# Kernel tuning notes

Measured on AMD Instinct MI355X. Metric: run time of the kernel, lower is better.

## Reference

```python
import jax, jax.numpy as jnp
import numpy as np

B = 16384       # batch of weight blocks
IN = 64         # input_size == e_dim
DENC = 512      # dim_encoder
NRES = 2        # n_resblock (weights shared, see ResidualStack [block]*n)
NE = 2048       # n_embeddings
P = 12          # basis vectors per block
BETA = 0.25
SCALE = 1.0
SHIFT = 0.0


def setup_inputs() -> dict:
    key = jax.random.key(0)
    ks = jax.random.split(key, 6)
    s = 0.02
    return {
        "x": jax.random.normal(ks[0], (B, IN), dtype=jnp.float32),
        "enc_w1": jax.random.normal(ks[1], (IN, DENC), dtype=jnp.float32) * s,
        "enc_b1": jnp.zeros((DENC,), jnp.float32),
        "res_w": jax.random.normal(ks[2], (DENC, DENC), dtype=jnp.float32) * s,
        "res_b": jnp.zeros((DENC,), jnp.float32),
        "res_g": jnp.ones((DENC,), jnp.float32),
        "res_beta": jnp.zeros((DENC,), jnp.float32),
        "enc_w2": jax.random.normal(ks[3], (DENC, IN * P), dtype=jnp.float32) * s,
        "enc_b2": jnp.zeros((IN * P,), jnp.float32),
        "emb": jax.random.uniform(ks[4], (NE, IN), jnp.float32, -1.0 / NE, 1.0 / NE),
    }


def _layer_norm(r, g, b):
    mu = jnp.mean(r, axis=-1, keepdims=True)
    var = jnp.mean((r - mu) ** 2, axis=-1, keepdims=True)
    return (r - mu) * jax.lax.rsqrt(var + 1e-5) * g + b


def reference(x, enc_w1, enc_b1, res_w, res_b, res_g, res_beta, enc_w2, enc_b2, emb):
    sg = jax.lax.stop_gradient
    x_shift = (x - SHIFT) / SCALE

    # encoder: Linear -> (shared ResBlock) x NRES -> Linear
    h = x_shift @ enc_w1 + enc_b1                      # (B, DENC)
    for _ in range(NRES):
        h = h + jax.nn.relu(_layer_norm(h @ res_w + res_b, res_g, res_beta))
    z = h @ enc_w2 + enc_b2                            # (B, P*IN)

    z_e = z.reshape(B, P, IN)
    zf = z_e.reshape(-1, IN)                           # (B*P, IN)

    # pairwise squared distances to codebook, argmin, gather
    d = (jnp.sum(zf ** 2, axis=1, keepdims=True)
         + jnp.sum(emb ** 2, axis=1)
         - 2.0 * zf @ emb.T)                           # (B*P, NE)
    idx = jnp.argmin(d, axis=1)                        # (B*P,)
    z_q = emb[idx].reshape(B, P, IN)

    loss = (jnp.mean((sg(z_q) - z_e) ** 2)
            + BETA * jnp.mean((z_q - sg(z_e)) ** 2))

    # straight-through estimator
    z_q = z_e + sg(z_q - z_e)

    counts = jnp.zeros((NE,), jnp.float32).at[idx].add(1.0) / idx.shape[0]
    perplexity = jnp.exp(-jnp.sum(counts * jnp.log(counts + 1e-10)))

    # pinv-based reconstruction: A (B, IN, P), coeff = pinv(A) @ x_shift
    A = jnp.transpose(z_q, (0, 2, 1))                  # (B, IN, P)
    coeff = jnp.matmul(jnp.linalg.pinv(A), x_shift[..., None])  # (B, P, 1)
    x_hat = jnp.matmul(A, coeff)[..., 0]               # (B, IN)
    x_hat = SCALE * x_hat + SHIFT

    return (loss, x_hat, perplexity, idx, coeff)
```

## Files before the change

kernel.cpp:

```cpp
#include <hip/hip_runtime.h>
#include <math.h>

#define B_    16384
#define IN_   64
#define DENC_ 512
#define NE_   2048
#define P_    12
#define ROWS_ 196608
#define BETA_ 0.25

#define XHAT_OFF 1
#define PERP_OFF 1048577
#define IDXF_OFF 1048578
#define COEF_OFF 1245186

typedef __bf16 bf16x8 __attribute__((ext_vector_type(8)));
typedef float  f32x16 __attribute__((ext_vector_type(16)));

__device__ __forceinline__ void split3(float v, __bf16& h, __bf16& m, __bf16& l) {
    h = (__bf16)v;
    float r1 = v - (float)h;
    m = (__bf16)r1;
    float r2 = r1 - (float)m;
    l = (__bf16)r2;
}

__device__ __forceinline__ void gload_lds16(const void* g, void* l) {
    __builtin_amdgcn_global_load_lds((const __attribute__((address_space(1))) void*)g,
                                     (__attribute__((address_space(3))) void*)l, 16, 0, 0);
}

__global__ void k_wsplit(const float* __restrict__ W,
                         __bf16* __restrict__ Wh, __bf16* __restrict__ Wm,
                         __bf16* __restrict__ Wl, int kshift, int N, int total) {
    int idx = blockIdx.x * 256 + threadIdx.x;
    if (idx < total) {
        int n = idx >> kshift;
        int k = idx & ((1 << kshift) - 1);
        float v = W[(size_t)k * N + n];
        __bf16 h, m, l;
        split3(v, h, m, l);
        Wh[idx] = h; Wm[idx] = m; Wl[idx] = l;
    }
}

__global__ __launch_bounds__(256, 2) void k_gemm_mfma(const float* __restrict__ A,
                                                      const __bf16* __restrict__ Bh,
                                                      const __bf16* __restrict__ Bm,
                                                      const __bf16* __restrict__ Bl,
                                                      const float* __restrict__ bias,
                                                      float* __restrict__ C,
                                                      int N, int K) {
    __shared__ __bf16 eS[2][3][64 * 64];

    const int nwg  = gridDim.x * gridDim.y;
    const int flat = blockIdx.y * gridDim.x + blockIdx.x;
    const int nf   = (flat & 7) * (nwg >> 3) + (flat >> 3);
    const int bx   = nf % gridDim.x;
    const int by   = nf / gridDim.x;

    const int tid = threadIdx.x;
    const int w = tid >> 6, lane = tid & 63;
    const int r0 = by * 256 + w * 64;
    const int n0 = bx * 64;
    const int lrow = lane & 31;
    const int half = lane >> 5;

    const int cc0 = tid >> 3, qq = tid & 7;
    const int cc1 = cc0 + 32;
    const size_t off0 = (size_t)cc0 * K + (size_t)((qq ^ (cc0 & 7)) * 8);
    const size_t off1 = (size_t)cc1 * K + (size_t)((qq ^ (cc1 & 7)) * 8);
    const size_t nbase = (size_t)n0 * K;
    const int ld0 = w * 512;
    const int ld1 = 2048 + w * 512;

    f32x16 acc00, acc01, acc10, acc11;
#pragma unroll
    for (int i = 0; i < 16; ++i) { acc00[i] = 0.0f; acc01[i] = 0.0f; acc10[i] = 0.0f; acc11[i] = 0.0f; }

    {
        const size_t b = nbase;
        gload_lds16(Bh + b + off0, &eS[0][0][ld0]);
        gload_lds16(Bh + b + off1, &eS[0][0][ld1]);
        gload_lds16(Bm + b + off0, &eS[0][1][ld0]);
        gload_lds16(Bm + b + off1, &eS[0][1][ld1]);
        gload_lds16(Bl + b + off0, &eS[0][2][ld0]);
        gload_lds16(Bl + b + off1, &eS[0][2][ld1]);
    }

    const int nch = K >> 6;
    for (int ch = 0; ch < nch; ++ch) {
        const int cur = ch & 1;
        __syncthreads();

        if (ch + 1 < nch) {
            const int nxt = cur ^ 1;
            const size_t b = nbase + (size_t)(ch + 1) * 64;
            gload_lds16(Bh + b + off0, &eS[nxt][0][ld0]);
            gload_lds16(Bh + b + off1, &eS[nxt][0][ld1]);
            gload_lds16(Bm + b + off0, &eS[nxt][1][ld0]);
            gload_lds16(Bm + b + off1, &eS[nxt][1][ld1]);
            gload_lds16(Bl + b + off0, &eS[nxt][2][ld0]);
            gload_lds16(Bl + b + off1, &eS[nxt][2][ld1]);
        }

        bf16x8 ah0[4], am0[4], al0[4], ah1[4], am1[4], al1[4];
        {
            const float* ar0 = A + (size_t)(r0 + lrow) * K + ch * 64 + half * 8;
            const float* ar1 = ar0 + (size_t)32 * K;
#pragma unroll
            for (int kc = 0; kc < 4; ++kc) {
                float4 u0 = *(const float4*)(ar0 + kc * 16);
                float4 u1 = *(const float4*)(ar0 + kc * 16 + 4);
                float va[8] = {u0.x, u0.y, u0.z, u0.w, u1.x, u1.y, u1.z, u1.w};
                float4 t0 = *(const float4*)(ar1 + kc * 16);
                float4 t1 = *(const float4*)(ar1 + kc * 16 + 4);
                float vb[8] = {t0.x, t0.y, t0.z, t0.w, t1.x, t1.y, t1.z, t1.w};
#pragma unroll
                for (int j = 0; j < 8; ++j) {
                    __bf16 hh, mm, ll;
                    split3(va[j], hh, mm, ll);
                    ah0[kc][j] = hh; am0[kc][j] = mm; al0[kc][j] = ll;
                    split3(vb[j], hh, mm, ll);
                    ah1[kc][j] = hh; am1[kc][j] = mm; al1[kc][j] = ll;
                }
            }
        }

#pragma unroll
        for (int kc = 0; kc < 4; ++kc) {
            const int q = kc * 2 + half;
            const int g = (q ^ (lrow & 7)) * 8;
            bf16x8 b0h = *(const bf16x8*)(&eS[cur][0][lrow * 64 + g]);
            bf16x8 b0m = *(const bf16x8*)(&eS[cur][1][lrow * 64 + g]);
            bf16x8 b0l = *(const bf16x8*)(&eS[cur][2][lrow * 64 + g]);
            bf16x8 b1h = *(const bf16x8*)(&eS[cur][0][(lrow + 32) * 64 + g]);
            bf16x8 b1m = *(const bf16x8*)(&eS[cur][1][(lrow + 32) * 64 + g]);
            bf16x8 b1l = *(const bf16x8*)(&eS[cur][2][(lrow + 32) * 64 + g]);

            acc00 = __builtin_amdgcn_mfma_f32_32x32x16_bf16(ah0[kc], b0h, acc00, 0, 0, 0);
            acc01 = __builtin_amdgcn_mfma_f32_32x32x16_bf16(ah0[kc], b1h, acc01, 0, 0, 0);
            acc10 = __builtin_amdgcn_mfma_f32_32x32x16_bf16(ah1[kc], b0h, acc10, 0, 0, 0);
            acc11 = __builtin_amdgcn_mfma_f32_32x32x16_bf16(ah1[kc], b1h, acc11, 0, 0, 0);
            acc00 = __builtin_amdgcn_mfma_f32_32x32x16_bf16(ah0[kc], b0m, acc00, 0, 0, 0);
            acc01 = __builtin_amdgcn_mfma_f32_32x32x16_bf16(ah0[kc], b1m, acc01, 0, 0, 0);
            acc10 = __builtin_amdgcn_mfma_f32_32x32x16_bf16(ah1[kc], b0m, acc10, 0, 0, 0);
            acc11 = __builtin_amdgcn_mfma_f32_32x32x16_bf16(ah1[kc], b1m, acc11, 0, 0, 0);
            acc00 = __builtin_amdgcn_mfma_f32_32x32x16_bf16(am0[kc], b0h, acc00, 0, 0, 0);
            acc01 = __builtin_amdgcn_mfma_f32_32x32x16_bf16(am0[kc], b1h, acc01, 0, 0, 0);
            acc10 = __builtin_amdgcn_mfma_f32_32x32x16_bf16(am1[kc], b0h, acc10, 0, 0, 0);
            acc11 = __builtin_amdgcn_mfma_f32_32x32x16_bf16(am1[kc], b1h, acc11, 0, 0, 0);
            acc00 = __builtin_amdgcn_mfma_f32_32x32x16_bf16(ah0[kc], b0l, acc00, 0, 0, 0);
            acc01 = __builtin_amdgcn_mfma_f32_32x32x16_bf16(ah0[kc], b1l, acc01, 0, 0, 0);
            acc10 = __builtin_amdgcn_mfma_f32_32x32x16_bf16(ah1[kc], b0l, acc10, 0, 0, 0);
            acc11 = __builtin_amdgcn_mfma_f32_32x32x16_bf16(ah1[kc], b1l, acc11, 0, 0, 0);
            acc00 = __builtin_amdgcn_mfma_f32_32x32x16_bf16(am0[kc], b0m, acc00, 0, 0, 0);
            acc01 = __builtin_amdgcn_mfma_f32_32x32x16_bf16(am0[kc], b1m, acc01, 0, 0, 0);
            acc10 = __builtin_amdgcn_mfma_f32_32x32x16_bf16(am1[kc], b0m, acc10, 0, 0, 0);
            acc11 = __builtin_amdgcn_mfma_f32_32x32x16_bf16(am1[kc], b1m, acc11, 0, 0, 0);
            acc00 = __builtin_amdgcn_mfma_f32_32x32x16_bf16(al0[kc], b0h, acc00, 0, 0, 0);
            acc01 = __builtin_amdgcn_mfma_f32_32x32x16_bf16(al0[kc], b1h, acc01, 0, 0, 0);
            acc10 = __builtin_amdgcn_mfma_f32_32x32x16_bf16(al1[kc], b0h, acc10, 0, 0, 0);
            acc11 = __builtin_amdgcn_mfma_f32_32x32x16_bf16(al1[kc], b1h, acc11, 0, 0, 0);
        }
    }

    const int col0 = n0 + lrow, col1 = col0 + 32;
    const float bv0 = bias[col0], bv1 = bias[col1];
#pragma unroll
    for (int r = 0; r < 16; ++r) {
        int rr = (r & 3) + 8 * (r >> 2) + 4 * half;
        C[(size_t)(r0 + rr) * N + col0] = acc00[r] + bv0;
        C[(size_t)(r0 + rr) * N + col1] = acc01[r] + bv1;
        C[(size_t)(r0 + 32 + rr) * N + col0] = acc10[r] + bv0;
        C[(size_t)(r0 + 32 + rr) * N + col1] = acc11[r] + bv1;
    }
}

__global__ __launch_bounds__(256) void k_lnrelu(const float* __restrict__ t,
                                                float* __restrict__ h,
                                                const float* __restrict__ g,
                                                const float* __restrict__ beta) {
    const int tid = threadIdx.x;
    const int wv = tid >> 6, lane = tid & 63;
    const int row = blockIdx.x * 4 + wv;
    const float* tr = t + (size_t)row * DENC_;
    float* hr = h + (size_t)row * DENC_;

    float4 v0 = *(const float4*)(tr + lane * 4);
    float4 v1 = *(const float4*)(tr + 256 + lane * 4);

    float s = v0.x + v0.y + v0.z + v0.w + v1.x + v1.y + v1.z + v1.w;
#pragma unroll
    for (int m = 1; m < 64; m <<= 1) s += __shfl_xor(s, m);
    float mu = s / 512.0f;

    float d0x = v0.x - mu, d0y = v0.y - mu, d0z = v0.z - mu, d0w = v0.w - mu;
    float d1x = v1.x - mu, d1y = v1.y - mu, d1z = v1.z - mu, d1w = v1.w - mu;
    float vs = d0x * d0x + d0y * d0y + d0z * d0z + d0w * d0w +
               d1x * d1x + d1y * d1y + d1z * d1z + d1w * d1w;
#pragma unroll
    for (int m = 1; m < 64; m <<= 1) vs += __shfl_xor(vs, m);
    float var = vs / 512.0f;
    float rs = (float)(1.0 / sqrt((double)var + 1e-5));

    float4 g0 = *(const float4*)(g + lane * 4);
    float4 g1 = *(const float4*)(g + 256 + lane * 4);
    float4 b0 = *(const float4*)(beta + lane * 4);
    float4 b1 = *(const float4*)(beta + 256 + lane * 4);

    float4 h0 = *(float4*)(hr + lane * 4);
    float4 h1 = *(float4*)(hr + 256 + lane * 4);

    h0.x += fmaxf(d0x * rs * g0.x + b0.x, 0.0f);
    h0.y += fmaxf(d0y * rs * g0.y + b0.y, 0.0f);
    h0.z += fmaxf(d0z * rs * g0.z + b0.z, 0.0f);
    h0.w += fmaxf(d0w * rs * g0.w + b0.w, 0.0f);
    h1.x += fmaxf(d1x * rs * g1.x + b1.x, 0.0f);
    h1.y += fmaxf(d1y * rs * g1.y + b1.y, 0.0f);
    h1.z += fmaxf(d1z * rs * g1.z + b1.z, 0.0f);
    h1.w += fmaxf(d1w * rs * g1.w + b1.w, 0.0f);

    *(float4*)(hr + lane * 4) = h0;
    *(float4*)(hr + 256 + lane * 4) = h1;
}

__global__ __launch_bounds__(256) void k_esplit_fast(const float* __restrict__ emb,
                                                     __bf16* __restrict__ Ehi,
                                                     __bf16* __restrict__ Emid,
                                                     __bf16* __restrict__ Elo) {
    const int wv = threadIdx.x >> 6, lane = threadIdx.x & 63;
    const int c = blockIdx.x * 4 + wv;
    float v = emb[(size_t)c * 64 + lane];
    __bf16 h, m, l;
    split3(v, h, m, l);
    Ehi[(size_t)c * 64 + lane] = h;
    Emid[(size_t)c * 64 + lane] = m;
    Elo[(size_t)c * 64 + lane] = l;
}

__global__ void k_esq(const float* __restrict__ emb, float* __restrict__ se) {
    int t = blockIdx.x * 256 + threadIdx.x;
    if (t < NE_) {
        float s = 0.0f;
        for (int k = 0; k < 64; ++k) {
            float v = emb[(size_t)t * 64 + k];
            s += v * v;
        }
        se[t] = s;
    }
}

__global__ __launch_bounds__(256) void k_rowsq(const float* __restrict__ z,
                                               float* __restrict__ sz) {
    const int tid = threadIdx.x;
    const int row = blockIdx.x * 64 + (tid >> 2);
    const int part = tid & 3;
    const float4* zp = (const float4*)(z + (size_t)row * 64) + part * 4;
    float s = 0.0f;
#pragma unroll
    for (int i = 0; i < 4; ++i) {
        float4 v = zp[i];
        s += v.x * v.x + v.y * v.y + v.z * v.z + v.w * v.w;
    }
    s += __shfl_xor(s, 1);
    s += __shfl_xor(s, 2);
    if (part == 0) sz[row] = s;
}

__global__ __launch_bounds__(256) void k_distm(const float* __restrict__ z,
                                               const float* __restrict__ se,
                                               const float* __restrict__ sz,
                                               const __bf16* __restrict__ Ehi,
                                               const __bf16* __restrict__ Emid,
                                               const __bf16* __restrict__ Elo,
                                               int* __restrict__ idxw,
                                               float* __restrict__ idxf,
                                               float* __restrict__ lossacc,
                                               int* __restrict__ counts) {
    __shared__ __bf16 eS[2][3][32 * 64];

    const int tid = threadIdx.x;
    const int w = tid >> 6, lane = tid & 63;
    const int r0 = blockIdx.x * 128 + w * 32;
    const int lrow = lane & 31;
    const int half = lane >> 5;

    const int cc = tid >> 3, qq = tid & 7;
    const int off = cc * 64 + (qq ^ (cc & 7)) * 8;
    const int ld = w * 512;

    bf16x8 ah[4], am[4], al[4];
    {
        const float* zr = z + (size_t)(r0 + lrow) * 64 + half * 8;
#pragma unroll
        for (int kc = 0; kc < 4; ++kc) {
            float4 u0 = *(const float4*)(zr + kc * 16);
            float4 u1 = *(const float4*)(zr + kc * 16 + 4);
            float v[8] = {u0.x, u0.y, u0.z, u0.w, u1.x, u1.y, u1.z, u1.w};
#pragma unroll
            for (int j = 0; j < 8; ++j) {
                __bf16 hh, mm, ll;
                split3(v[j], hh, mm, ll);
                ah[kc][j] = hh; am[kc][j] = mm; al[kc][j] = ll;
            }
        }
    }

    float szv[16];
#pragma unroll
    for (int r = 0; r < 16; ++r) {
        int rl = (r & 3) + 8 * (r >> 2) + 4 * half;
        szv[r] = sz[r0 + rl];
    }

    float bd[16];
    int bi[16];
#pragma unroll
    for (int r = 0; r < 16; ++r) { bd[r] = 1e30f; bi[r] = 0; }

    gload_lds16(Ehi + off, &eS[0][0][ld]);
    gload_lds16(Emid + off, &eS[0][1][ld]);
    gload_lds16(Elo + off, &eS[0][2][ld]);

    for (int ch = 0; ch < 64; ++ch) {
        const int cur = ch & 1;
        __syncthreads();

        if (ch + 1 < 64) {
            const int nxt = cur ^ 1;
            const int b = (ch + 1) * 2048;
            gload_lds16(Ehi + b + off, &eS[nxt][0][ld]);
            gload_lds16(Emid + b + off, &eS[nxt][1][ld]);
            gload_lds16(Elo + b + off, &eS[nxt][2][ld]);
        }

        f32x16 acc;
#pragma unroll
        for (int i = 0; i < 16; ++i) acc[i] = 0.0f;

#pragma unroll
        for (int kc = 0; kc < 4; ++kc) {
            const int q = kc * 2 + half;
            const int g = (q ^ (lrow & 7)) * 8;
            bf16x8 bh = *(const bf16x8*)(&eS[cur][0][lrow * 64 + g]);
            bf16x8 bm = *(const bf16x8*)(&eS[cur][1][lrow * 64 + g]);
            bf16x8 bl = *(const bf16x8*)(&eS[cur][2][lrow * 64 + g]);

            acc = __builtin_amdgcn_mfma_f32_32x32x16_bf16(ah[kc], bh, acc, 0, 0, 0);
            acc = __builtin_amdgcn_mfma_f32_32x32x16_bf16(ah[kc], bm, acc, 0, 0, 0);
            acc = __builtin_amdgcn_mfma_f32_32x32x16_bf16(am[kc], bh, acc, 0, 0, 0);
            acc = __builtin_amdgcn_mfma_f32_32x32x16_bf16(ah[kc], bl, acc, 0, 0, 0);
            acc = __builtin_amdgcn_mfma_f32_32x32x16_bf16(am[kc], bm, acc, 0, 0, 0);
            acc = __builtin_amdgcn_mfma_f32_32x32x16_bf16(al[kc], bh, acc, 0, 0, 0);
        }

        const int c0 = ch * 32;
        const float se0 = se[c0 + lrow];
        const int   ci0 = c0 + lrow;
#pragma unroll
        for (int r = 0; r < 16; ++r) {
            float d0 = fmaf(-2.0f, acc[r], szv[r] + se0);
            if (d0 < bd[r]) { bd[r] = d0; bi[r] = ci0; }
        }
    }

#pragma unroll
    for (int r = 0; r < 16; ++r) {
        float d = bd[r];
        int i = bi[r];
#pragma unroll
        for (int off2 = 1; off2 < 32; off2 <<= 1) {
            float od = __shfl_xor(d, off2);
            int oi = __shfl_xor(i, off2);
            if (od < d || (od == d && oi < i)) { d = od; i = oi; }
        }
        bd[r] = d; bi[r] = i;
    }

    if (lrow == 0) {
        float lsum = 0.0f;
#pragma unroll
        for (int r = 0; r < 16; ++r) {
            int rl = (r & 3) + 8 * (r >> 2) + 4 * half;
            int row = r0 + rl;
            idxw[row] = bi[r];
            idxf[row] = (float)bi[r];
            lsum += bd[r];
            atomicAdd(&counts[bi[r]], 1);
        }
        atomicAdd(lossacc, lsum);
    }
}

__global__ __launch_bounds__(256) void k_lossperp(const float* __restrict__ lossacc,
                                                  const int* __restrict__ counts,
                                                  float* __restrict__ out) {
    __shared__ double red[256];
    const int tid = threadIdx.x;

    double hsum = 0.0;
    for (int i = tid; i < NE_; i += 256) {
        float p = (float)counts[i] / 196608.0f;
        float lg = logf(p + 1e-10f);
        hsum += (double)(p * lg);
    }
    red[tid] = hsum;
    __syncthreads();
    for (int off = 128; off > 0; off >>= 1) {
        if (tid < off) red[tid] += red[tid + off];
        __syncthreads();
    }
    if (tid == 0) {
        out[PERP_OFF] = (float)exp(-red[0]);
        out[0] = (float)((double)lossacc[0] * (1.0 + BETA_) / ((double)ROWS_ * IN_));
    }
}

__global__ __launch_bounds__(64) void k_pinv(const float* __restrict__ xin,
                                             const float* __restrict__ emb,
                                             const int* __restrict__ idxw,
                                             float* __restrict__ coeff,
                                             float* __restrict__ xhat) {
    __shared__ float aS[12][65];
    __shared__ float xS[64];
    __shared__ double GS[12][12];
    __shared__ double bS[12];
    __shared__ double yS[12];
    __shared__ double uS[12];
    __shared__ float cS[12];

    const int lane = threadIdx.x;
    const int b = blockIdx.x;

    int my = 0;
    if (lane < 12) my = idxw[(size_t)b * 12 + lane];
    int id[12];
#pragma unroll
    for (int p = 0; p < 12; ++p) id[p] = __shfl(my, p);

    int rep = lane, mcnt = 1;
    if (lane < 12) {
        rep = -1;
        mcnt = 0;
        for (int q = 0; q < 12; ++q) {
            if (id[q] == id[lane]) {
                if (rep < 0) rep = q;
                mcnt++;
            }
        }
    }

#pragma unroll
    for (int p = 0; p < 12; ++p) aS[p][lane] = emb[(size_t)id[p] * 64 + lane];
    xS[lane] = xin[(size_t)b * 64 + lane];
    __syncthreads();

    for (int item = lane; item < 90; item += 64) {
        if (item < 78) {
            int j = 0, k = 0, c = item;
            for (j = 0; j < 12; ++j) {
                int cnt = 12 - j;
                if (c < cnt) { k = j + c; break; }
                c -= cnt;
            }
            double s = 0.0;
            for (int t = 0; t < 64; ++t) s += (double)aS[j][t] * (double)aS[k][t];
            GS[j][k] = s;
            GS[k][j] = s;
        } else {
            int j = item - 78;
            double s = 0.0;
            for (int t = 0; t < 64; ++t) s += (double)aS[j][t] * (double)xS[t];
            bS[j] = s;
        }
    }
    __syncthreads();

    if (lane == 0) {
        for (int p = 0; p < 12; ++p) {
            int rp = -1;
            for (int q = 0; q < 12; ++q) {
                if (id[q] == id[p]) { rp = q; break; }
            }
            if (rp != p) {
                for (int q = 0; q < 12; ++q) {
                    GS[p][q] = 0.0;
                    GS[q][p] = 0.0;
                }
                GS[p][p] = 1.0;
                bS[p] = 0.0;
            }
        }
    }
    __syncthreads();

    for (int j = 0; j < 12; ++j) {
        if (lane == j) {
            double s = GS[j][j];
            for (int k = 0; k < j; ++k) {
                double l = GS[j][k];
                s -= l * l;
            }
            GS[j][j] = sqrt(fmax(s, 1e-30));
        }
        __syncthreads();
        if (lane > j && lane < 12) {
            double s = GS[lane][j];
            for (int k = 0; k < j; ++k) s -= GS[lane][k] * GS[j][k];
            GS[lane][j] = s / GS[j][j];
        }
        __syncthreads();
    }

    double s = (lane < 12) ? bS[lane] : 0.0;
    for (int k = 0; k < 12; ++k) {
        if (lane == k) yS[k] = s / GS[k][k];
        __syncthreads();
        double yk = yS[k];
        if (lane > k && lane < 12) s -= GS[lane][k] * yk;
    }
    double tacc = 0.0;
    for (int k = 11; k >= 0; --k) {
        if (lane == k) uS[k] = (yS[k] - tacc) / GS[k][k];
        __syncthreads();
        double uk = uS[k];
        if (lane < k) tacc += GS[k][lane] * uk;
    }
    __syncthreads();

    if (lane < 12) {
        double c = uS[rep] / (double)mcnt;
        coeff[(size_t)b * 12 + lane] = (float)c;
        cS[lane] = (float)c;
    }
    __syncthreads();

    float sx = 0.0f;
#pragma unroll
    for (int p = 0; p < 12; ++p) sx += aS[p][lane] * cS[p];
    xhat[(size_t)b * 64 + lane] = sx;
}


extern "C" void kernel_launch(void* const* d_in, const int* in_sizes, int n_in,
                              void* d_out, int out_size, void* d_ws, size_t ws_size,
                              hipStream_t stream) {
    const float* x        = (const float*)d_in[0];
    const float* enc_w1   = (const float*)d_in[1];
    const float* enc_b1   = (const float*)d_in[2];
    const float* res_w    = (const float*)d_in[3];
    const float* res_b    = (const float*)d_in[4];
    const float* res_g    = (const float*)d_in[5];
    const float* res_beta = (const float*)d_in[6];
    const float* enc_w2   = (const float*)d_in[7];
    const float* enc_b2   = (const float*)d_in[8];
    const float* emb      = (const float*)d_in[9];

    float* out = (float*)d_out;

    float* h  = (float*)d_ws;
    float* tz = h + (size_t)B_ * DENC_;
    float* se    = h;
    float* sz    = h + 2048;
    int*   idxw  = (int*)(h + 2048 + (size_t)ROWS_);
    int*   cnts  = (int*)(h + 2048 + 2 * (size_t)ROWS_);
    float* lossacc = (float*)(cnts + NE_);
    __bf16* Ehi  = (__bf16*)(h + 2048 + 2 * (size_t)ROWS_ + 2048 + 16);
    __bf16* Emid = Ehi + (size_t)NE_ * 64;
    __bf16* Elo  = Emid + (size_t)NE_ * 64;
    __bf16* W1h = (__bf16*)(tz + (size_t)B_ * 768);
    __bf16* W1m = W1h + (size_t)DENC_ * IN_;
    __bf16* W1l = W1m + (size_t)DENC_ * IN_;
    __bf16* Wrh = W1l + (size_t)DENC_ * IN_;
    __bf16* Wrm = Wrh + (size_t)DENC_ * DENC_;
    __bf16* Wrl = Wrm + (size_t)DENC_ * DENC_;
    __bf16* W2h = Wrl + (size_t)DENC_ * DENC_;
    __bf16* W2m = W2h + (size_t)768 * DENC_;
    __bf16* W2l = W2m + (size_t)768 * DENC_;

    float* t = tz;
    float* z = tz;

    k_wsplit<<<(DENC_ * IN_ + 255) / 256, 256, 0, stream>>>(enc_w1, W1h, W1m, W1l, 6, DENC_, DENC_ * IN_);
    k_wsplit<<<(DENC_ * DENC_ + 255) / 256, 256, 0, stream>>>(res_w, Wrh, Wrm, Wrl, 9, DENC_, DENC_ * DENC_);
    k_wsplit<<<(768 * DENC_ + 255) / 256, 256, 0, stream>>>(enc_w2, W2h, W2m, W2l, 9, 768, 768 * DENC_);

    k_gemm_mfma<<<dim3(DENC_ / 64, B_ / 256), 256, 0, stream>>>(x, W1h, W1m, W1l, enc_b1, h, DENC_, IN_);
    for (int r = 0; r < 2; ++r) {
        k_gemm_mfma<<<dim3(DENC_ / 64, B_ / 256), 256, 0, stream>>>(h, Wrh, Wrm, Wrl, res_b, t, DENC_, DENC_);
        k_lnrelu<<<B_ / 4, 256, 0, stream>>>(t, h, res_g, res_beta);
    }
    k_gemm_mfma<<<dim3(768 / 64, B_ / 256), 256, 0, stream>>>(h, W2h, W2m, W2l, enc_b2, z, 768, DENC_);

    hipMemsetAsync(cnts, 0, (NE_ + 16) * sizeof(int), stream);
    k_esplit_fast<<<NE_ / 4, 256, 0, stream>>>(emb, Ehi, Emid, Elo);
    k_esq<<<NE_ / 256, 256, 0, stream>>>(emb, se);
    k_rowsq<<<ROWS_ / 64, 256, 0, stream>>>(z, sz);
    k_distm<<<ROWS_ / 128, 256, 0, stream>>>(z, se, sz, Ehi, Emid, Elo,
                                             idxw, out + IDXF_OFF, lossacc, cnts);
    k_lossperp<<<1, 256, 0, stream>>>(lossacc, cnts, out);
    k_pinv<<<B_, 64, 0, stream>>>(x, emb, idxw, out + COEF_OFF, out + XHAT_OFF);
}
```

Before: 705.3 us.

## Pre-split activations to bf16 triplets and use a linear LDS layout in distm

Adds a k_asplit kernel that converts each fp32 activation matrix once into hi/mid/lo bf16 planes. A new GEMM variant, k_gemm_mfma_p, then loads those planes directly instead of re-splitting fp32 inputs inside every column-block workgroup. This is meant to remove split arithmetic that is repeated across the 8–12 column tiles, at the cost of extra launches and about 50% more bytes per activation element (6 instead of 4). Separately, the distance kernel's codebook staging in LDS changes from an XOR-swizzled layout to a linear layout where each lane reads consecutive chunks, aiming to simplify addressing and avoid bank conflicts.

Result: slower. 811.4 us (+15.0%).

```diff
diff --git a/kernel.cpp b/kernel.cpp
--- a/kernel.cpp
+++ b/kernel.cpp
@@ -42,6 +42,26 @@
         split3(v, h, m, l);
         Wh[idx] = h; Wm[idx] = m; Wl[idx] = l;
     }
+}
+
+__global__ __launch_bounds__(256) void k_asplit(const float* __restrict__ A,
+                                                __bf16* __restrict__ Ah,
+                                                __bf16* __restrict__ Am,
+                                                __bf16* __restrict__ Al) {
+    size_t i = ((size_t)blockIdx.x * 256 + threadIdx.x) * 8;
+    float4 u0 = *(const float4*)(A + i);
+    float4 u1 = *(const float4*)(A + i + 4);
+    float v[8] = {u0.x, u0.y, u0.z, u0.w, u1.x, u1.y, u1.z, u1.w};
+    bf16x8 ph, pm, pl;
+#pragma unroll
+    for (int j = 0; j < 8; ++j) {
+        __bf16 hh, mm, ll;
+        split3(v[j], hh, mm, ll);
+        ph[j] = hh; pm[j] = mm; pl[j] = ll;
+    }
+    *(bf16x8*)(Ah + i) = ph;
+    *(bf16x8*)(Am + i) = pm;
+    *(bf16x8*)(Al + i) = pl;
 }
 
 __global__ __launch_bounds__(256, 2) void k_gemm_mfma(const float* __restrict__ A,
@@ -177,6 +197,133 @@
     }
 }
 
+__global__ __launch_bounds__(256, 2) void k_gemm_mfma_p(const __bf16* __restrict__ Ah,
+                                                        const __bf16* __restrict__ Am,
+                                                        const __bf16* __restrict__ Al,
+                                                        const __bf16* __restrict__ Bh,
+                                                        const __bf16* __restrict__ Bm,
+                                                        const __bf16* __restrict__ Bl,
+                                                        const float* __restrict__ bias,
+                                                        float* __restrict__ C,
+                                                        int N, int K) {
+    __shared__ __bf16 eS[2][3][64 * 64];
+
+    const int nwg  = gridDim.x * gridDim.y;
+    const int flat = blockIdx.y * gridDim.x + blockIdx.x;
+    const int nf   = (flat & 7) * (nwg >> 3) + (flat >> 3);
+    const int bx   = nf % gridDim.x;
+    const int by   = nf / gridDim.x;
+
+    const int tid = threadIdx.x;
+    const int w = tid >> 6, lane = tid & 63;
+    const int r0 = by * 256 + w * 64;
+    const int n0 = bx * 64;
+    const int lrow = lane & 31;
+    const int half = lane >> 5;
+
+    const int cc0 = tid >> 3, qq = tid & 7;
+    const int cc1 = cc0 + 32;
+    const size_t off0 = (size_t)cc0 * K + (size_t)((qq ^ (cc0 & 7)) * 8);
+    const size_t off1 = (size_t)cc1 * K + (size_t)((qq ^ (cc1 & 7)) * 8);
+    const size_t nbase = (size_t)n0 * K;
+    const int ld0 = w * 512;
+    const int ld1 = 2048 + w * 512;
+
+    f32x16 acc00, acc01, acc10, acc11;
+#pragma unroll
+    for (int i = 0; i < 16; ++i) { acc00[i] = 0.0f; acc01[i] = 0.0f; acc10[i] = 0.0f; acc11[i] = 0.0f; }
+
+    {
+        const size_t b = nbase;
+        gload_lds16(Bh + b + off0, &eS[0][0][ld0]);
+        gload_lds16(Bh + b + off1, &eS[0][0][ld1]);
+        gload_lds16(Bm + b + off0, &eS[0][1][ld0]);
+        gload_lds16(Bm + b + off1, &eS[0][1][ld1]);
+        gload_lds16(Bl + b + off0, &eS[0][2][ld0]);
+        gload_lds16(Bl + b + off1, &eS[0][2][ld1]);
+    }
+
+    const int nch = K >> 6;
+    for (int ch = 0; ch < nch; ++ch) {
+        const int cur = ch & 1;
+        __syncthreads();
+
+        if (ch + 1 < nch) {
+            const int nxt = cur ^ 1;
+            const size_t b = nbase + (size_t)(ch + 1) * 64;
+            gload_lds16(Bh + b + off0, &eS[nxt][0][ld0]);
+            gload_lds16(Bh + b + off1, &eS[nxt][0][ld1]);
+            gload_lds16(Bm + b + off0, &eS[nxt][1][ld0]);
+            gload_lds16(Bm + b + off1, &eS[nxt][1][ld1]);
+            gload_lds16(Bl + b + off0, &eS[nxt][2][ld0]);
+            gload_lds16(Bl + b + off1, &eS[nxt][2][ld1]);
+        }
+
+        bf16x8 ah0[4], am0[4], al0[4], ah1[4], am1[4], al1[4];
+        {
+            const size_t base0 = (size_t)(r0 + lrow) * K + ch * 64 + half * 8;
+            const size_t base1 = base0 + (size_t)32 * K;
+#pragma unroll
+            for (int kc = 0; kc < 4; ++kc) {
+                ah0[kc] = *(const bf16x8*)(Ah + base0 + kc * 16);
+                am0[kc] = *(const bf16x8*)(Am + base0 + kc * 16);
+                al0[kc] = *(const bf16x8*)(Al + base0 + kc * 16);
+                ah1[kc] = *(const bf16x8*)(Ah + base1 + kc * 16);
+                am1[kc] = *(const bf16x8*)(Am + base1 + kc * 16);
+                al1[kc] = *(const bf16x8*)(Al + base1 + kc * 16);
+            }
+        }
+
+#pragma unroll
+        for (int kc = 0; kc < 4; ++kc) {
+            const int q = kc * 2 + half;
+            const int g = (q ^ (lrow & 7)) * 8;
+            bf16x8 b0h = *(const bf16x8*)(&eS[cur][0][lrow * 64 + g]);
+            bf16x8 b0m = *(const bf16x8*)(&eS[cur][1][lrow * 64 + g]);
+            bf16x8 b0l = *(const bf16x8*)(&eS[cur][2][lrow * 64 + g]);
+            bf16x8 b1h = *(const bf16x8*)(&eS[cur][0][(lrow + 32) * 64 + g]);
+            bf16x8 b1m = *(const bf16x8*)(&eS[cur][1][(lrow + 32) * 64 + g]);
+            bf16x8 b1l = *(const bf16x8*)(&eS[cur][2][(lrow + 32) * 64 + g]);
+
+            acc00 = __builtin_amdgcn_mfma_f32_32x32x16_bf16(ah0[kc], b0h, acc00, 0, 0, 0);
+            acc01 = __builtin_amdgcn_mfma_f32_32x32x16_bf16(ah0[kc], b1h, acc01, 0, 0, 0);
+            acc10 = __builtin_amdgcn_mfma_f32_32x32x16_bf16(ah1[kc], b0h, acc10, 0, 0, 0);
+            acc11 = __builtin_amdgcn_mfma_f32_32x32x16_bf16(ah1[kc], b1h, acc11, 0, 0, 0);
+            acc00 = __builtin_amdgcn_mfma_f32_32x32x16_bf16(ah0[kc], b0m, acc00, 0, 0, 0);
+            acc01 = __builtin_amdgcn_mfma_f32_32x32x16_bf16(ah0[kc], b1m, acc01, 0, 0, 0);
+            acc10 = __builtin_amdgcn_mfma_f32_32x32x16_bf16(ah1[kc], b0m, acc10, 0, 0, 0);
+            acc11 = __builtin_amdgcn_mfma_f32_32x32x16_bf16(ah1[kc], b1m, acc11, 0, 0, 0);
+            acc00 = __builtin_amdgcn_mfma_f32_32x32x16_bf16(am0[kc], b0h, acc00, 0, 0, 0);
+            acc01 = __builtin_amdgcn_mfma_f32_32x32x16_bf16(am0[kc], b1h, acc01, 0, 0, 0);
+            acc10 = __builtin_amdgcn_mfma_f32_32x32x16_bf16(am1[kc], b0h, acc10, 0, 0, 0);
+            acc11 = __builtin_amdgcn_mfma_f32_32x32x16_bf16(am1[kc], b1h, acc11, 0, 0, 0);
+            acc00 = __builtin_amdgcn_mfma_f32_32x32x16_bf16(ah0[kc], b0l, acc00, 0, 0, 0);
+            acc01 = __builtin_amdgcn_mfma_f32_32x32x16_bf16(ah0[kc], b1l, acc01, 0, 0, 0);
+            acc10 = __builtin_amdgcn_mfma_f32_32x32x16_bf16(ah1[kc], b0l, acc10, 0, 0, 0);
+            acc11 = __builtin_amdgcn_mfma_f32_32x32x16_bf16(ah1[kc], b1l, acc11, 0, 0, 0);
+            acc00 = __builtin_amdgcn_mfma_f32_32x32x16_bf16(am0[kc], b0m, acc00, 0, 0, 0);
+            acc01 = __builtin_amdgcn_mfma_f32_32x32x16_bf16(am0[kc], b1m, acc01, 0, 0, 0);
+            acc10 = __builtin_amdgcn_mfma_f32_32x32x16_bf16(am1[kc], b0m, acc10, 0, 0, 0);
+            acc11 = __builtin_amdgcn_mfma_f32_32x32x16_bf16(am1[kc], b1m, acc11, 0, 0, 0);
+            acc00 = __builtin_amdgcn_mfma_f32_32x32x16_bf16(al0[kc], b0h, acc00, 0, 0, 0);
+            acc01 = __builtin_amdgcn_mfma_f32_32x32x16_bf16(al0[kc], b1h, acc01, 0, 0, 0);
+            acc10 = __builtin_amdgcn_mfma_f32_32x32x16_bf16(al1[kc], b0h, acc10, 0, 0, 0);
+            acc11 = __builtin_amdgcn_mfma_f32_32x32x16_bf16(al1[kc], b1h, acc11, 0, 0, 0);
+        }
+    }
+
+    const int col0 = n0 + lrow, col1 = col0 + 32;
+    const float bv0 = bias[col0], bv1 = bias[col1];
+#pragma unroll
+    for (int r = 0; r < 16; ++r) {
+        int rr = (r & 3) + 8 * (r >> 2) + 4 * half;
+        C[(size_t)(r0 + rr) * N + col0] = acc00[r] + bv0;
+        C[(size_t)(r0 + rr) * N + col1] = acc01[r] + bv1;
+        C[(size_t)(r0 + 32 + rr) * N + col0] = acc10[r] + bv0;
+        C[(size_t)(r0 + 32 + rr) * N + col1] = acc11[r] + bv1;
+    }
+}
+
 __global__ __launch_bounds__(256) void k_lnrelu(const float* __restrict__ t,
                                                 float* __restrict__ h,
                                                 const float* __restrict__ g,
@@ -286,8 +433,7 @@
     const int lrow = lane & 31;
     const int half = lane >> 5;
 
-    const int cc = tid >> 3, qq = tid & 7;
-    const int off = cc * 64 + (qq ^ (cc & 7)) * 8;
+    const int off = (tid & 31) * 64 + ((tid >> 5) & 1) * 8 + (tid >> 6) * 16;
     const int ld = w * 512;
 
     bf16x8 ah[4], am[4], al[4];
@@ -342,10 +488,10 @@
 #pragma unroll
         for (int kc = 0; kc < 4; ++kc) {
             const int q = kc * 2 + half;
-            const int g = (q ^ (lrow & 7)) * 8;
-            bf16x8 bh = *(const bf16x8*)(&eS[cur][0][lrow * 64 + g]);
-            bf16x8 bm = *(const bf16x8*)(&eS[cur][1][lrow * 64 + g]);
-            bf16x8 bl = *(const bf16x8*)(&eS[cur][2][lrow * 64 + g]);
+            const int e = q * 256 + lrow * 8;
+            bf16x8 bh = *(const bf16x8*)(&eS[cur][0][e]);
+            bf16x8 bm = *(const bf16x8*)(&eS[cur][1][e]);
+            bf16x8 bl = *(const bf16x8*)(&eS[cur][2][e]);
 
             acc = __builtin_amdgcn_mfma_f32_32x32x16_bf16(ah[kc], bh, acc, 0, 0, 0);
             acc = __builtin_amdgcn_mfma_f32_32x32x16_bf16(ah[kc], bm, acc, 0, 0, 0);
@@ -578,6 +724,9 @@
     __bf16* W2h = Wrl + (size_t)DENC_ * DENC_;
     __bf16* W2m = W2h + (size_t)768 * DENC_;
     __bf16* W2l = W2m + (size_t)768 * DENC_;
+    __bf16* Ahp = W2l + (size_t)768 * DENC_;
+    __bf16* Amp = Ahp + (size_t)B_ * DENC_;
+    __bf16* Alp = Amp + (size_t)B_ * DENC_;
 
     float* t = tz;
     float* z = tz;
@@ -587,11 +736,15 @@
     k_wsplit<<<(768 * DENC_ + 255) / 256, 256, 0, stream>>>(enc_w2, W2h, W2m, W2l, 9, 768, 768 * DENC_);
 
     k_gemm_mfma<<<dim3(DENC_ / 64, B_ / 256), 256, 0, stream>>>(x, W1h, W1m, W1l, enc_b1, h, DENC_, IN_);
+    k_asplit<<<(B_ * DENC_) / (256 * 8), 256, 0, stream>>>(h, Ahp, Amp, Alp);
     for (int r = 0; r < 2; ++r) {
-        k_gemm_mfma<<<dim3(DENC_ / 64, B_ / 256), 256, 0, stream>>>(h, Wrh, Wrm, Wrl, res_b, t, DENC_, DENC_);
+        k_gemm_mfma_p<<<dim3(DENC_ / 64, B_ / 256), 256, 0, stream>>>(Ahp, Amp, Alp, Wrh, Wrm, Wrl,
+                                                                      res_b, t, DENC_, DENC_);
         k_lnrelu<<<B_ / 4, 256, 0, stream>>>(t, h, res_g, res_beta);
-    }
-    k_gemm_mfma<<<dim3(768 / 64, B_ / 256), 256, 0, stream>>>(h, W2h, W2m, W2l, enc_b2, z, 768, DENC_);
+        k_asplit<<<(B_ * DENC_) / (256 * 8), 256, 0, stream>>>(h, Ahp, Amp, Alp);
+    }
+    k_gemm_mfma_p<<<dim3(768 / 64, B_ / 256), 256, 0, stream>>>(Ahp, Amp, Alp, W2h, W2m, W2l,
+                                                                enc_b2, z, 768, DENC_);
 
     hipMemsetAsync(cnts, 0, (NE_ + 16) * sizeof(int), stream);
     k_esplit_fast<<<NE_ / 4, 256, 0, stream>>>(emb, Ehi, Emid, Elo);
```
